# Optimization experiments

Measured on AMD Instinct MI355X. Metric: run time of the kernel, lower is better.

## Reference

```python
import jax, jax.numpy as jnp
import numpy as np

BETA = 0.25

def setup_inputs() -> dict:
    key = jax.random.key(0)
    k1, k2 = jax.random.split(key)
    z = jax.random.normal(k1, (32, 256, 32, 32), dtype=jnp.float32)
    # embedding init ~ U(-1/K, 1/K) as intended by the module
    K, D = 1024, 256
    codebook = jax.random.uniform(k2, (K, D), dtype=jnp.float32, minval=-1.0 / K, maxval=1.0 / K)
    return {"z": z, "codebook": codebook}


def reference(z, codebook):
    # z: [B, D, H, W] -> [B, H, W, D]
    zt = jnp.transpose(z, (0, 2, 3, 1))
    B, H, W, D = zt.shape
    z_flat = zt.reshape(-1, D)  # [N, D]
    # pairwise squared distance: ||z||^2 + ||e||^2 - 2 z e^T
    dist = (
        jnp.sum(z_flat * z_flat, axis=1, keepdims=True)
        + jnp.sum(codebook * codebook, axis=1)[None, :]
        - 2.0 * jnp.matmul(z_flat, codebook.T)
    )  # [N, K]
    idx = jnp.argmin(dist, axis=1)  # [N]
    z_q = codebook[idx].reshape(B, H, W, D)
    sg = jax.lax.stop_gradient
    loss = jnp.mean((sg(z_q) - zt) ** 2) + BETA * jnp.mean((sg(zt) - z_q) ** 2)
    # straight-through estimator
    z_q = zt + sg(z_q - zt)
    z_q = jnp.transpose(z_q, (0, 3, 1, 2))  # back to [B, D, H, W]
    return z_q, idx, loss
```

## Files before the change

### kernel.cpp

```cpp
#include <hip/hip_runtime.h>


#define D_DIM   256
#define K_CODES 1024
#define HW      1024
#define MT      64
#define NT      512
#define BK      4
#define THREADS 512
#define NSTEP   128

#define ZQ_OFF   0
#define IDX_OFF  8388608
#define LOSS_OFF 8421376

#define SMEM_FLOATS (BK*NT + MT + MT)
#define SMEM_BYTES  (SMEM_FLOATS * 4)

extern __shared__ float smem[];

__global__ void enorm_kernel(const float* __restrict__ cb, float* __restrict__ enorm) {
    int gt = blockIdx.x * blockDim.x + threadIdx.x;
    int k = gt >> 6;
    int lane = gt & 63;
    const float4* row = (const float4*)(cb + (size_t)k * D_DIM);
    float4 v = row[lane];
    float s = fmaf(v.x, v.x, fmaf(v.y, v.y, fmaf(v.z, v.z, v.w * v.w)));
    #pragma unroll
    for (int off = 32; off; off >>= 1) s += __shfl_xor(s, off);
    if (lane == 0) enorm[k] = s;
}

__global__ __launch_bounds__(THREADS, 2)
void vq_kernel(
        const float* __restrict__ z, const float* __restrict__ cb,
        const float* __restrict__ enorm, float* __restrict__ out)
{
    float* Es      = smem;
    float* znorm_s = smem + BK * NT;
    int*   bestm   = (int*)(smem + BK * NT + MT);

    const int t   = threadIdx.x;
    const int blk = blockIdx.x;
    const int b   = blk >> 4;
    const int p0  = (blk & 15) * MT;
    const float* zb = z + (size_t)b * D_DIM * HW;

    const float* cbp = cb + (size_t)t * D_DIM;

    float4 sv = *(const float4*)(cbp);

    {
        int m = t & (MT - 1), q = t >> 6;
        const float* col = zb + p0 + m;
        double zp = 0.0;
        #pragma unroll 8
        for (int d = q * 32; d < q * 32 + 32; ++d) {
            double v = (double)col[(size_t)d * HW];
            zp += v * v;
        }
        double* zscr = (double*)Es;
        zscr[q * MT + m] = zp;
    }
    __syncthreads();
    if (t < MT) {
        double* zscr = (double*)Es;
        double s = 0.0;
        #pragma unroll
        for (int q = 0; q < 8; ++q) s += zscr[q * MT + t];
        znorm_s[t] = (float)s;
    }

    const int tx = t & 63;
    const int m_base = (t >> 6) * 8;
    const int kx4 = tx * 4;

    float bestv[8]; int besti[8];
    #pragma unroll
    for (int i = 0; i < 8; ++i) { bestv[i] = 3.4e38f; besti[i] = 0; }

    float acc[8][8];
    #pragma unroll
    for (int i = 0; i < 8; ++i)
        #pragma unroll
        for (int j = 0; j < 8; ++j) acc[i][j] = 0.f;

    for (int g = 0; g < NSTEP; ++g) {
        const int c = g >> 6, s = g & 63;
        const int dk = s * BK;

        float a[BK][8];
        #pragma unroll
        for (int dd = 0; dd < BK; ++dd) {
            const int uoff = __builtin_amdgcn_readfirstlane((dk + dd) * HW + p0 + m_base);
            const float* ar = zb + uoff;
            #pragma unroll
            for (int i = 0; i < 8; ++i) a[dd][i] = ar[i];
        }

        __syncthreads();
        Es[0 * NT + t] = sv.x;
        Es[1 * NT + t] = sv.y;
        Es[2 * NT + t] = sv.z;
        Es[3 * NT + t] = sv.w;

        {
            const int gn = (g < NSTEP - 1) ? g + 1 : NSTEP - 1;
            sv = *(const float4*)(cbp + (((size_t)(gn >> 6)) << 17) + ((gn & 63) << 2));
        }
        __syncthreads();

        #pragma unroll
        for (int dd = 0; dd < BK; ++dd) {
            float e[8];
            const float* Er = Es + dd * NT + kx4;
            *(float4*)(e)     = *(const float4*)(Er);
            *(float4*)(e + 4) = *(const float4*)(Er + 256);
            #pragma unroll
            for (int i = 0; i < 8; ++i)
                #pragma unroll
                for (int j = 0; j < 8; ++j)
                    acc[i][j] = fmaf(a[dd][i], e[j], acc[i][j]);
        }

        if (s == 63) {
            #pragma unroll
            for (int j = 0; j < 8; ++j) {
                const int kidx = c * NT + ((j < 4) ? (kx4 + j) : (252 + kx4 + j));
                const float bn = enorm[kidx];
                #pragma unroll
                for (int i = 0; i < 8; ++i) {
                    float A   = znorm_s[m_base + i] + bn;
                    float val = A - 2.0f * acc[i][j];
                    if (val < bestv[i] || (val == bestv[i] && kidx < besti[i])) {
                        bestv[i] = val; besti[i] = kidx;
                    }
                }
            }
            #pragma unroll
            for (int i = 0; i < 8; ++i)
                #pragma unroll
                for (int j = 0; j < 8; ++j) acc[i][j] = 0.f;
        }
    }

    #pragma unroll
    for (int i = 0; i < 8; ++i) {
        float v = bestv[i]; int ix = besti[i];
        #pragma unroll
        for (int off = 32; off; off >>= 1) {
            float ov = __shfl_xor(v, off);
            int   oi = __shfl_xor(ix, off);
            if (ov < v || (ov == v && oi < ix)) { v = ov; ix = oi; }
        }
        if (tx == 0) {
            bestm[m_base + i] = ix;
            out[IDX_OFF + (size_t)blk * MT + m_base + i] = (float)ix;
        }
    }
    __syncthreads();

    float lsum = 0.f;
    const size_t zq_base = (size_t)b * D_DIM * HW + p0;
    for (int i2 = t; i2 < D_DIM * MT / 4; i2 += THREADS) {
        int p = i2 & (MT - 1), d4 = i2 >> 6;
        int idx = bestm[p];
        float4 cv = *(const float4*)(cb + (size_t)idx * D_DIM + d4 * 4);
        const float* zp = zb + p0 + p;
        float z0 = zp[(size_t)(d4 * 4 + 0) * HW];
        float z1 = zp[(size_t)(d4 * 4 + 1) * HW];
        float z2 = zp[(size_t)(d4 * 4 + 2) * HW];
        float z3 = zp[(size_t)(d4 * 4 + 3) * HW];
        float e0 = cv.x - z0, e1 = cv.y - z1, e2 = cv.z - z2, e3 = cv.w - z3;
        lsum = fmaf(e0, e0, lsum); lsum = fmaf(e1, e1, lsum);
        lsum = fmaf(e2, e2, lsum); lsum = fmaf(e3, e3, lsum);
        out[zq_base + (size_t)(d4 * 4 + 0) * HW + p] = cv.x;
        out[zq_base + (size_t)(d4 * 4 + 1) * HW + p] = cv.y;
        out[zq_base + (size_t)(d4 * 4 + 2) * HW + p] = cv.z;
        out[zq_base + (size_t)(d4 * 4 + 3) * HW + p] = cv.w;
    }
    #pragma unroll
    for (int off = 32; off; off >>= 1) lsum += __shfl_xor(lsum, off);
    __syncthreads();
    if ((t & 63) == 0) Es[t >> 6] = lsum;
    __syncthreads();
    if (t == 0) {
        float s = 0.f;
        #pragma unroll
        for (int w = 0; w < 8; ++w) s += Es[w];
        atomicAdd(out + LOSS_OFF, s * (1.25f / 8388608.f));
    }
}

extern "C" void kernel_launch(void* const* d_in, const int* in_sizes, int n_in,
                              void* d_out, int out_size, void* d_ws, size_t ws_size,
                              hipStream_t stream) {
    const float* z  = (const float*)d_in[0];
    const float* cb = (const float*)d_in[1];
    float* out = (float*)d_out;
    float* enorm = (float*)d_ws;

    hipMemsetAsync(out + LOSS_OFF, 0, sizeof(float), stream);

    enorm_kernel<<<256, 256, 0, stream>>>(cb, enorm);

    hipFuncSetAttribute((const void*)vq_kernel,
                        hipFuncAttributeMaxDynamicSharedMemorySize, SMEM_BYTES);
    vq_kernel<<<512, THREADS, SMEM_BYTES, stream>>>(z, cb, enorm, out);
}
```

Before: 304.3 us.

## Double-buffer codebook tile in LDS with deeper prefetch and BK=8

Doubles the K-slice per step from 4 to 8 and ping-pongs the shared-memory codebook tile between two buffers, so each iteration writes the next tile while computing on the current one with a single barrier instead of two. Codebook register prefetch is moved two steps ahead, and the z operand is now read directly from global inside the FMA loop rather than staged into a register array first. This is meant to halve barrier count and hide global-load latency, at the cost of twice the LDS footprint and more live registers, which may reduce occupancy at the two-blocks-per-CU launch bound.

```diff
diff --git a/kernel.cpp b/kernel.cpp
--- a/kernel.cpp
+++ b/kernel.cpp
@@ -6,15 +6,15 @@
 #define HW      1024
 #define MT      64
 #define NT      512
-#define BK      4
+#define BK      8
 #define THREADS 512
-#define NSTEP   128
+#define NSTEP   64
 
 #define ZQ_OFF   0
 #define IDX_OFF  8388608
 #define LOSS_OFF 8421376
 
-#define SMEM_FLOATS (BK*NT + MT + MT)
+#define SMEM_FLOATS (2*BK*NT + MT + MT)
 #define SMEM_BYTES  (SMEM_FLOATS * 4)
 
 extern __shared__ float smem[];
@@ -37,8 +37,8 @@
         const float* __restrict__ enorm, float* __restrict__ out)
 {
     float* Es      = smem;
-    float* znorm_s = smem + BK * NT;
-    int*   bestm   = (int*)(smem + BK * NT + MT);
+    float* znorm_s = smem + 2 * BK * NT;
+    int*   bestm   = (int*)(smem + 2 * BK * NT + MT);
 
     const int t   = threadIdx.x;
     const int blk = blockIdx.x;
@@ -48,7 +48,8 @@
 
     const float* cbp = cb + (size_t)t * D_DIM;
 
-    float4 sv = *(const float4*)(cbp);
+    float4 s0a = *(const float4*)(cbp);
+    float4 s0b = *(const float4*)(cbp + 4);
 
     {
         int m = t & (MT - 1), q = t >> 6;
@@ -70,6 +71,17 @@
         for (int q = 0; q < 8; ++q) s += zscr[q * MT + t];
         znorm_s[t] = (float)s;
     }
+    __syncthreads();
+
+    {
+        Es[0 * NT + t] = s0a.x;  Es[1 * NT + t] = s0a.y;
+        Es[2 * NT + t] = s0a.z;  Es[3 * NT + t] = s0a.w;
+        Es[4 * NT + t] = s0b.x;  Es[5 * NT + t] = s0b.y;
+        Es[6 * NT + t] = s0b.z;  Es[7 * NT + t] = s0b.w;
+    }
+    float4 svA = *(const float4*)(cbp + BK);
+    float4 svB = *(const float4*)(cbp + BK + 4);
+    __syncthreads();
 
     const int tx = t & 63;
     const int m_base = (t >> 6) * 8;
@@ -85,45 +97,41 @@
         #pragma unroll
         for (int j = 0; j < 8; ++j) acc[i][j] = 0.f;
 
+    int cur = 0;
     for (int g = 0; g < NSTEP; ++g) {
-        const int c = g >> 6, s = g & 63;
-        const int dk = s * BK;
-
-        float a[BK][8];
+        if (g < NSTEP - 1) {
+            float* En = Es + (cur ^ 1) * (BK * NT);
+            En[0 * NT + t] = svA.x;  En[1 * NT + t] = svA.y;
+            En[2 * NT + t] = svA.z;  En[3 * NT + t] = svA.w;
+            En[4 * NT + t] = svB.x;  En[5 * NT + t] = svB.y;
+            En[6 * NT + t] = svB.z;  En[7 * NT + t] = svB.w;
+        }
+        {
+            const int gn = (g + 2 < NSTEP) ? g + 2 : NSTEP - 1;
+            const float* p = cbp + (((size_t)(gn >> 5)) << 17) + ((gn & 31) << 3);
+            svA = *(const float4*)(p);
+            svB = *(const float4*)(p + 4);
+        }
+
+        const int dk = (g & 31) * BK;
+        const float* Ec = Es + cur * (BK * NT);
         #pragma unroll
         for (int dd = 0; dd < BK; ++dd) {
             const int uoff = __builtin_amdgcn_readfirstlane((dk + dd) * HW + p0 + m_base);
             const float* ar = zb + uoff;
-            #pragma unroll
-            for (int i = 0; i < 8; ++i) a[dd][i] = ar[i];
-        }
-
-        __syncthreads();
-        Es[0 * NT + t] = sv.x;
-        Es[1 * NT + t] = sv.y;
-        Es[2 * NT + t] = sv.z;
-        Es[3 * NT + t] = sv.w;
-
-        {
-            const int gn = (g < NSTEP - 1) ? g + 1 : NSTEP - 1;
-            sv = *(const float4*)(cbp + (((size_t)(gn >> 6)) << 17) + ((gn & 63) << 2));
-        }
-        __syncthreads();
-
-        #pragma unroll
-        for (int dd = 0; dd < BK; ++dd) {
             float e[8];
-            const float* Er = Es + dd * NT + kx4;
+            const float* Er = Ec + dd * NT + kx4;
             *(float4*)(e)     = *(const float4*)(Er);
             *(float4*)(e + 4) = *(const float4*)(Er + 256);
             #pragma unroll
             for (int i = 0; i < 8; ++i)
                 #pragma unroll
                 for (int j = 0; j < 8; ++j)
-                    acc[i][j] = fmaf(a[dd][i], e[j], acc[i][j]);
-        }
-
-        if (s == 63) {
+                    acc[i][j] = fmaf(ar[i], e[j], acc[i][j]);
+        }
+
+        if ((g & 31) == 31) {
+            const int c = g >> 5;
             #pragma unroll
             for (int j = 0; j < 8; ++j) {
                 const int kidx = c * NT + ((j < 4) ? (kx4 + j) : (252 + kx4 + j));
@@ -142,6 +150,8 @@
                 #pragma unroll
                 for (int j = 0; j < 8; ++j) acc[i][j] = 0.f;
         }
+        __syncthreads();
+        cur ^= 1;
     }
 
     #pragma unroll
```

Result: faster. 284.0 us (-6.7%).

## Use split-bf16 MFMA distances with candidate list and exact fp32 rescoring

Applied to the files above, without the earlier changes.

Replaces the scalar FP32 FMA distance GEMM with bf16x3 split MFMA (hi*hi + hi*lo + lo*hi) on matrix cores. Near-minimum candidates within an error margin go into a shared list and are rescored with an exact fp32 dot product to keep argmin ties correct. The z tile is staged once in LDS and reused for the loss pass. The change adds large LDS use that lowers occupancy, plus serial exact rescoring, and falls back to a full exact pass if the list overflows.

```diff
diff --git a/kernel.cpp b/kernel.cpp
--- a/kernel.cpp
+++ b/kernel.cpp
@@ -1,23 +1,41 @@
 #include <hip/hip_runtime.h>
+#include <stdint.h>
 
 
 #define D_DIM   256
-#define K_CODES 1024
 #define HW      1024
 #define MT      64
-#define NT      512
-#define BK      4
 #define THREADS 512
-#define NSTEP   128
+#define LIST_CAP 2048
 
 #define ZQ_OFF   0
 #define IDX_OFF  8388608
 #define LOSS_OFF 8421376
 
-#define SMEM_FLOATS (BK*NT + MT + MT)
-#define SMEM_BYTES  (SMEM_FLOATS * 4)
-
-extern __shared__ float smem[];
+typedef __attribute__((ext_vector_type(8))) short  short8;
+typedef __attribute__((ext_vector_type(4))) float  f32x4;
+typedef __attribute__((ext_vector_type(4))) unsigned int u32x4;
+
+#define ZFP_ROW   264
+#define OFF_ZFP   0
+#define OFF_HEB   67584
+#define OFF_LEB   83968
+#define OFF_HZA   100352
+#define OFF_LZA   104448
+#define OFF_LIST  108544
+#define OFF_ZN    116736
+#define OFF_DLT   116992
+#define OFF_RMIN  117248
+#define OFF_RBV   117504
+#define OFF_RBK   117760
+#define OFF_BESTM 118016
+#define OFF_CNT   118272
+#define OFF_OVF   118276
+#define SMEM_BYTES 118288
+
+#define SWZ(rowi, u16) (((u16) ^ ((((rowi) >> 1) & 3) << 4)))
+
+extern __shared__ char smc[];
 
 __global__ void enorm_kernel(const float* __restrict__ cb, float* __restrict__ enorm) {
     int gt = blockIdx.x * blockDim.x + threadIdx.x;
@@ -31,14 +49,53 @@
     if (lane == 0) enorm[k] = s;
 }
 
+__device__ __forceinline__ void split2(float a, float b, unsigned &hi, unsigned &lo) {
+    unsigned ba = __float_as_uint(a), bb = __float_as_uint(b);
+    unsigned ha = ba & 0xFFFF0000u, hb = bb & 0xFFFF0000u;
+    float ra = a - __uint_as_float(ha);
+    float rb = b - __uint_as_float(hb);
+    hi = (ha >> 16) | hb;
+    lo = (__float_as_uint(ra) >> 16) | (__float_as_uint(rb) & 0xFFFF0000u);
+}
+
+__device__ __forceinline__ void split8(const float* src, u32x4 &hv, u32x4 &lv) {
+    f32x4 A0 = *(const f32x4*)(src);
+    f32x4 A1 = *(const f32x4*)(src + 4);
+    unsigned h0, l0, h1, l1, h2, l2, h3, l3;
+    split2(A0.x, A0.y, h0, l0);
+    split2(A0.z, A0.w, h1, l1);
+    split2(A1.x, A1.y, h2, l2);
+    split2(A1.z, A1.w, h3, l3);
+    hv.x = h0; hv.y = h1; hv.z = h2; hv.w = h3;
+    lv.x = l0; lv.y = l1; lv.z = l2; lv.w = l3;
+}
+
+__device__ __noinline__ float exact_val(const char* sm, const float* cb,
+                                        const float* enorm, int m, int k) {
+    const float* zr = (const float*)(sm + OFF_ZFP) + (size_t)m * ZFP_ROW;
+    const float* cr = cb + (size_t)k * D_DIM;
+    float dot = 0.f;
+    #pragma unroll 8
+    for (int d = 0; d < D_DIM; ++d) dot = fmaf(zr[d], cr[d], dot);
+    float A = ((const float*)(sm + OFF_ZN))[m] + enorm[k];
+    return A - 2.0f * dot;
+}
+
 __global__ __launch_bounds__(THREADS, 2)
-void vq_kernel(
-        const float* __restrict__ z, const float* __restrict__ cb,
-        const float* __restrict__ enorm, float* __restrict__ out)
+void vq_kernel(const float* __restrict__ z, const float* __restrict__ cb,
+               const float* __restrict__ enorm, float* __restrict__ out)
 {
-    float* Es      = smem;
-    float* znorm_s = smem + BK * NT;
-    int*   bestm   = (int*)(smem + BK * NT + MT);
+    char* sm = smc;
+    float*    zfp   = (float*)(sm + OFF_ZFP);
+    float*    znS   = (float*)(sm + OFF_ZN);
+    float*    dltS  = (float*)(sm + OFF_DLT);
+    unsigned* rminU = (unsigned*)(sm + OFF_RMIN);
+    unsigned* rbv   = (unsigned*)(sm + OFF_RBV);
+    unsigned* rbk   = (unsigned*)(sm + OFF_RBK);
+    int*      bestm = (int*)(sm + OFF_BESTM);
+    unsigned* listU = (unsigned*)(sm + OFF_LIST);
+    int*      cntP  = (int*)(sm + OFF_CNT);
+    int*      ovfP  = (int*)(sm + OFF_OVF);
 
     const int t   = threadIdx.x;
     const int blk = blockIdx.x;
@@ -46,117 +103,179 @@
     const int p0  = (blk & 15) * MT;
     const float* zb = z + (size_t)b * D_DIM * HW;
 
-    const float* cbp = cb + (size_t)t * D_DIM;
-
-    float4 sv = *(const float4*)(cbp);
+    #pragma unroll
+    for (int r = 0; r < 8; ++r) {
+        int d = (t >> 4) + r * 32;
+        int m4 = (t & 15) * 4;
+        f32x4 v = *(const f32x4*)(zb + (size_t)d * HW + p0 + m4);
+        zfp[(m4 + 0) * ZFP_ROW + d] = v.x;
+        zfp[(m4 + 1) * ZFP_ROW + d] = v.y;
+        zfp[(m4 + 2) * ZFP_ROW + d] = v.z;
+        zfp[(m4 + 3) * ZFP_ROW + d] = v.w;
+    }
+    __syncthreads();
 
     {
-        int m = t & (MT - 1), q = t >> 6;
-        const float* col = zb + p0 + m;
+        int m = t & 63, q = t >> 6;
+        const float* zr = zfp + m * ZFP_ROW + q * 32;
         double zp = 0.0;
         #pragma unroll 8
-        for (int d = q * 32; d < q * 32 + 32; ++d) {
-            double v = (double)col[(size_t)d * HW];
-            zp += v * v;
-        }
-        double* zscr = (double*)Es;
-        zscr[q * MT + m] = zp;
-    }
-    __syncthreads();
-    if (t < MT) {
-        double* zscr = (double*)Es;
+        for (int d = 0; d < 32; ++d) { double v = (double)zr[d]; zp += v * v; }
+        double* zscr = (double*)(sm + OFF_HEB);
+        zscr[q * 64 + m] = zp;
+    }
+    __syncthreads();
+    if (t < 64) {
+        double* zscr = (double*)(sm + OFF_HEB);
         double s = 0.0;
         #pragma unroll
-        for (int q = 0; q < 8; ++q) s += zscr[q * MT + t];
-        znorm_s[t] = (float)s;
-    }
-
-    const int tx = t & 63;
-    const int m_base = (t >> 6) * 8;
-    const int kx4 = tx * 4;
-
-    float bestv[8]; int besti[8];
-    #pragma unroll
-    for (int i = 0; i < 8; ++i) { bestv[i] = 3.4e38f; besti[i] = 0; }
-
-    float acc[8][8];
-    #pragma unroll
-    for (int i = 0; i < 8; ++i)
-        #pragma unroll
-        for (int j = 0; j < 8; ++j) acc[i][j] = 0.f;
-
-    for (int g = 0; g < NSTEP; ++g) {
-        const int c = g >> 6, s = g & 63;
-        const int dk = s * BK;
-
-        float a[BK][8];
-        #pragma unroll
-        for (int dd = 0; dd < BK; ++dd) {
-            const int uoff = __builtin_amdgcn_readfirstlane((dk + dd) * HW + p0 + m_base);
-            const float* ar = zb + uoff;
-            #pragma unroll
-            for (int i = 0; i < 8; ++i) a[dd][i] = ar[i];
-        }
-
+        for (int q = 0; q < 8; ++q) s += zscr[q * 64 + t];
+        float zn = (float)s;
+        znS[t]  = zn;
+        dltS[t] = 1.15e-5f * sqrtf(zn) + 9.5e-5f;
+        rbv[t]  = 0x7f800000u;
+        rbk[t]  = 0xFFFFFFFFu;
+    }
+    if (t == 0) { *cntP = 0; *ovfP = 0; }
+    __syncthreads();
+
+    const int l   = t & 63;
+    const int wid = t >> 6;
+    const int wm  = wid & 3;
+    const int wc  = wid >> 2;
+    const int l15 = l & 15;
+
+    for (int kc = 0; kc < 4; ++kc) {
+        if (t < 64) rminU[t] = 0x7f800000u;
+
+        f32x4 acc[8];
+        #pragma unroll
+        for (int sc = 0; sc < 8; ++sc) acc[sc] = (f32x4){0.f, 0.f, 0.f, 0.f};
+
+        for (int s = 0; s < 8; ++s) {
+            const int d0 = s * 32;
+            __syncthreads();
+
+            #pragma unroll
+            for (int i = 0; i < 2; ++i) {
+                int id = i * 512 + t;
+                int u = id & 3, code = id >> 2;
+                const float* src = cb + (size_t)(kc * 256 + code) * D_DIM + d0 + u * 8;
+                u32x4 hv, lv;
+                split8(src, hv, lv);
+                int off = code * 64 + SWZ(code, u * 16);
+                *(u32x4*)(sm + OFF_HEB + off) = hv;
+                *(u32x4*)(sm + OFF_LEB + off) = lv;
+            }
+            {
+                int m = (t >> 2) & 63, u = t & 3, arr = t >> 8;
+                const float* zr = zfp + m * ZFP_ROW + d0 + u * 8;
+                u32x4 hv, lv;
+                split8(zr, hv, lv);
+                int off = m * 64 + SWZ(m, u * 16);
+                *(u32x4*)(sm + (arr ? OFF_LZA : OFF_HZA) + off) = arr ? lv : hv;
+            }
+            __syncthreads();
+
+            int arow = wm * 16 + l15;
+            int aoff = arow * 64 + SWZ(arow, (l >> 4) * 16);
+            short8 hzF = *(const short8*)(sm + OFF_HZA + aoff);
+            short8 lzF = *(const short8*)(sm + OFF_LZA + aoff);
+            #pragma unroll
+            for (int c4 = 0; c4 < 2; ++c4) {
+                short8 he[4], le[4];
+                #pragma unroll
+                for (int j = 0; j < 4; ++j) {
+                    int codeL = wc * 128 + (c4 * 4 + j) * 16 + l15;
+                    int boff = codeL * 64 + SWZ(codeL, (l >> 4) * 16);
+                    he[j] = *(const short8*)(sm + OFF_HEB + boff);
+                    le[j] = *(const short8*)(sm + OFF_LEB + boff);
+                }
+                #pragma unroll
+                for (int j = 0; j < 4; ++j)
+                    acc[c4*4+j] = __builtin_amdgcn_mfma_f32_16x16x32_bf16(hzF, he[j], acc[c4*4+j], 0, 0, 0);
+                #pragma unroll
+                for (int j = 0; j < 4; ++j)
+                    acc[c4*4+j] = __builtin_amdgcn_mfma_f32_16x16x32_bf16(hzF, le[j], acc[c4*4+j], 0, 0, 0);
+                #pragma unroll
+                for (int j = 0; j < 4; ++j)
+                    acc[c4*4+j] = __builtin_amdgcn_mfma_f32_16x16x32_bf16(lzF, he[j], acc[c4*4+j], 0, 0, 0);
+            }
+        }
+
+        float bn[8];
+        #pragma unroll
+        for (int sc = 0; sc < 8; ++sc)
+            bn[sc] = enorm[kc * 256 + wc * 128 + sc * 16 + l15];
+
+        #pragma unroll
+        for (int reg = 0; reg < 4; ++reg) {
+            int row = wm * 16 + (l >> 4) * 4 + reg;
+            float zn = znS[row];
+            float vmin = 3.4e38f;
+            #pragma unroll
+            for (int sc = 0; sc < 8; ++sc) {
+                float val = (zn + bn[sc]) - 2.0f * acc[sc][reg];
+                vmin = fminf(vmin, val);
+            }
+            #pragma unroll
+            for (int off = 8; off; off >>= 1) vmin = fminf(vmin, __shfl_xor(vmin, off));
+            if (l15 == 0) atomicMin(&rminU[row], __float_as_uint(vmin));
+        }
         __syncthreads();
-        Es[0 * NT + t] = sv.x;
-        Es[1 * NT + t] = sv.y;
-        Es[2 * NT + t] = sv.z;
-        Es[3 * NT + t] = sv.w;
-
-        {
-            const int gn = (g < NSTEP - 1) ? g + 1 : NSTEP - 1;
-            sv = *(const float4*)(cbp + (((size_t)(gn >> 6)) << 17) + ((gn & 63) << 2));
+
+        #pragma unroll
+        for (int reg = 0; reg < 4; ++reg) {
+            int row = wm * 16 + (l >> 4) * 4 + reg;
+            float thr = __uint_as_float(rminU[row]) + dltS[row];
+            float zn = znS[row];
+            #pragma unroll
+            for (int sc = 0; sc < 8; ++sc) {
+                float val = (zn + bn[sc]) - 2.0f * acc[sc][reg];
+                if (val <= thr) {
+                    int slot = atomicAdd(cntP, 1);
+                    int kg = kc * 256 + wc * 128 + sc * 16 + l15;
+                    if (slot < LIST_CAP) listU[slot] = ((unsigned)row << 16) | (unsigned)kg;
+                    else *ovfP = 1;
+                }
+            }
         }
         __syncthreads();
-
-        #pragma unroll
-        for (int dd = 0; dd < BK; ++dd) {
-            float e[8];
-            const float* Er = Es + dd * NT + kx4;
-            *(float4*)(e)     = *(const float4*)(Er);
-            *(float4*)(e + 4) = *(const float4*)(Er + 256);
-            #pragma unroll
-            for (int i = 0; i < 8; ++i)
-                #pragma unroll
-                for (int j = 0; j < 8; ++j)
-                    acc[i][j] = fmaf(a[dd][i], e[j], acc[i][j]);
-        }
-
-        if (s == 63) {
-            #pragma unroll
-            for (int j = 0; j < 8; ++j) {
-                const int kidx = c * NT + ((j < 4) ? (kx4 + j) : (252 + kx4 + j));
-                const float bn = enorm[kidx];
-                #pragma unroll
-                for (int i = 0; i < 8; ++i) {
-                    float A   = znorm_s[m_base + i] + bn;
-                    float val = A - 2.0f * acc[i][j];
-                    if (val < bestv[i] || (val == bestv[i] && kidx < besti[i])) {
-                        bestv[i] = val; besti[i] = kidx;
-                    }
-                }
-            }
-            #pragma unroll
-            for (int i = 0; i < 8; ++i)
-                #pragma unroll
-                for (int j = 0; j < 8; ++j) acc[i][j] = 0.f;
-        }
-    }
-
-    #pragma unroll
-    for (int i = 0; i < 8; ++i) {
-        float v = bestv[i]; int ix = besti[i];
-        #pragma unroll
-        for (int off = 32; off; off >>= 1) {
-            float ov = __shfl_xor(v, off);
-            int   oi = __shfl_xor(ix, off);
-            if (ov < v || (ov == v && oi < ix)) { v = ov; ix = oi; }
-        }
-        if (tx == 0) {
-            bestm[m_base + i] = ix;
-            out[IDX_OFF + (size_t)blk * MT + m_base + i] = (float)ix;
-        }
+    }
+
+    const int n = min(*cntP, LIST_CAP);
+    const int isovf = *ovfP;
+    if (!isovf) {
+        for (int i = t; i < n; i += THREADS) {
+            unsigned e = listU[i];
+            float val = exact_val(sm, cb, enorm, (int)(e >> 16), (int)(e & 0xFFFFu));
+            atomicMin(&rbv[e >> 16], __float_as_uint(val));
+        }
+        __syncthreads();
+        for (int i = t; i < n; i += THREADS) {
+            unsigned e = listU[i];
+            int m = (int)(e >> 16), k = (int)(e & 0xFFFFu);
+            float val = exact_val(sm, cb, enorm, m, k);
+            if (__float_as_uint(val) == rbv[m]) atomicMin(&rbk[m], (unsigned)k);
+        }
+    } else {
+        for (int id = t; id < MT * 1024; id += THREADS) {
+            float val = exact_val(sm, cb, enorm, id >> 10, id & 1023);
+            atomicMin(&rbv[id >> 10], __float_as_uint(val));
+        }
+        __syncthreads();
+        for (int id = t; id < MT * 1024; id += THREADS) {
+            int m = id >> 10, k = id & 1023;
+            float val = exact_val(sm, cb, enorm, m, k);
+            if (__float_as_uint(val) == rbv[m]) atomicMin(&rbk[m], (unsigned)k);
+        }
+    }
+    __syncthreads();
+
+    if (t < 64) {
+        int k = (int)rbk[t];
+        bestm[t] = k;
+        out[IDX_OFF + (size_t)blk * MT + t] = (float)k;
     }
     __syncthreads();
 
@@ -165,12 +284,9 @@
     for (int i2 = t; i2 < D_DIM * MT / 4; i2 += THREADS) {
         int p = i2 & (MT - 1), d4 = i2 >> 6;
         int idx = bestm[p];
-        float4 cv = *(const float4*)(cb + (size_t)idx * D_DIM + d4 * 4);
-        const float* zp = zb + p0 + p;
-        float z0 = zp[(size_t)(d4 * 4 + 0) * HW];
-        float z1 = zp[(size_t)(d4 * 4 + 1) * HW];
-        float z2 = zp[(size_t)(d4 * 4 + 2) * HW];
-        float z3 = zp[(size_t)(d4 * 4 + 3) * HW];
+        f32x4 cv = *(const f32x4*)(cb + (size_t)idx * D_DIM + d4 * 4);
+        const float* zr = zfp + p * ZFP_ROW + d4 * 4;
+        float z0 = zr[0], z1 = zr[1], z2 = zr[2], z3 = zr[3];
         float e0 = cv.x - z0, e1 = cv.y - z1, e2 = cv.z - z2, e3 = cv.w - z3;
         lsum = fmaf(e0, e0, lsum); lsum = fmaf(e1, e1, lsum);
         lsum = fmaf(e2, e2, lsum); lsum = fmaf(e3, e3, lsum);
@@ -182,12 +298,13 @@
     #pragma unroll
     for (int off = 32; off; off >>= 1) lsum += __shfl_xor(lsum, off);
     __syncthreads();
-    if ((t & 63) == 0) Es[t >> 6] = lsum;
+    float* lscr = (float*)(sm + OFF_LIST);
+    if ((t & 63) == 0) lscr[t >> 6] = lsum;
     __syncthreads();
     if (t == 0) {
         float s = 0.f;
         #pragma unroll
-        for (int w = 0; w < 8; ++w) s += Es[w];
+        for (int w = 0; w < 8; ++w) s += lscr[w];
         atomicAdd(out + LOSS_OFF, s * (1.25f / 8388608.f));
     }
 }
```

Result: faster. 273.5 us (-10.1%).
